# Kernel tuning notes

Measured on AMD Instinct MI355X. Metric: run time of the kernel, lower is better.

Reference implementation:

```python
import jax, jax.numpy as jnp
import numpy as np

N_NODES = 50000
N_EDGES = 1200000
NODE_DIM = 64
HIDDEN = 64
OUT_DIM = 1
N_LAYERS = 3


def setup_inputs() -> dict:
    key = jax.random.key(0)
    ks = jax.random.split(key, 16)
    inp = {
        "H": jax.random.normal(ks[0], (N_NODES, NODE_DIM), dtype=jnp.float32),
        "edge_index": jax.random.randint(ks[1], (2, N_EDGES), 0, N_NODES, dtype=jnp.int64),
        "E": jax.random.normal(ks[2], (N_EDGES, 16), dtype=jnp.float32),
    }
    # per-layer params: node_encoder (enc) and update_w (upd); weights stored [in, out]
    for i in range(N_LAYERS):
        in_dim = NODE_DIM if i == 0 else HIDDEN
        s = 1.0 / np.sqrt(in_dim)
        inp[f"enc_w{i}"] = jax.random.uniform(ks[3 + 2 * i], (in_dim, HIDDEN), jnp.float32, -s, s)
        inp[f"enc_b{i}"] = jax.random.uniform(ks[4 + 2 * i], (HIDDEN,), jnp.float32, -s, s)
        sh = 1.0 / np.sqrt(HIDDEN)
        inp[f"upd_w{i}"] = jax.random.uniform(ks[9 + 2 * i], (HIDDEN, HIDDEN), jnp.float32, -sh, sh)
        inp[f"upd_b{i}"] = jax.random.uniform(ks[10 + 2 * i], (HIDDEN,), jnp.float32, -sh, sh)
    so = 1.0 / np.sqrt(HIDDEN)
    inp["out_w"] = jax.random.uniform(ks[15], (HIDDEN, OUT_DIM), jnp.float32, -so, so)
    inp["out_b"] = jnp.zeros((OUT_DIM,), jnp.float32)
    return inp


def _gcn_forward(H, edge_index, params):
    u, v = edge_index[0], edge_index[1]
    # symmetric normalization with implicit self-loop degree bump (calc_norm_factor)
    deg = jax.ops.segment_sum(jnp.ones(u.shape[0], H.dtype), u, num_segments=N_NODES) + 1.0
    dis = deg ** -0.5  # deg >= 1, never inf
    norm = dis[u] * dis[v]  # [n_edges]
    for i in range(N_LAYERS):
        enc_w, enc_b, upd_w, upd_b = params[i]
        H = H @ enc_w + enc_b                      # node_encoder
        msgs = norm[:, None] * H[u]                # gather + scale
        agg = jax.ops.segment_sum(msgs, v, num_segments=N_NODES)  # scatter-add
        H = jax.nn.relu((agg + H) @ upd_w + upd_b)  # update + ReLU (dropout = identity in eval)
    return H


def reference(H, edge_index, E, enc_w0, enc_b0, upd_w0, upd_b0, enc_w1, enc_b1,
              upd_w1, upd_b1, enc_w2, enc_b2, upd_w2, upd_b2, out_w, out_b):
    params = [(enc_w0, enc_b0, upd_w0, upd_b0),
              (enc_w1, enc_b1, upd_w1, upd_b1),
              (enc_w2, enc_b2, upd_w2, upd_b2)]
    Hf = _gcn_forward(H, edge_index, params)
    graph_emb = jnp.mean(Hf, axis=0, keepdims=True)  # [1, HIDDEN] readout (batch=None)
    return graph_emb @ out_w + out_b                 # [1, OUT_DIM]
```

## Files before the change

### kernel.cpp

```cpp
#include <hip/hip_runtime.h>
#include <hip/hip_fp16.h>

#define NN 50000
#define NE 1200000
#define DIM 64
#define NB 782
#define SLICES 512
#define ES 2344
#define VCAP 2048
#define GB 782
#define FRONT_LDS 33792

__global__ __launch_bounds__(256) void k_fold(const float* __restrict__ E0, const float* __restrict__ e0,
                                              const float* __restrict__ U0, const float* __restrict__ ub0,
                                              const float* __restrict__ E1, const float* __restrict__ e1,
                                              const float* __restrict__ U1, const float* __restrict__ ub1,
                                              const float* __restrict__ E2, const float* __restrict__ e2,
                                              const float* __restrict__ U2, const float* __restrict__ ub2,
                                              float* __restrict__ Wp, float* __restrict__ cvec,
                                              float* __restrict__ dvec) {
    __shared__ float Es[64][64];
    __shared__ float Us[64][64];
    int i = blockIdx.x;
    const float* E  = (i == 0) ? E0  : (i == 1) ? E1  : E2;
    const float* e  = (i == 0) ? e0  : (i == 1) ? e1  : e2;
    const float* U  = (i == 0) ? U0  : (i == 1) ? U1  : U2;
    const float* ub = (i == 0) ? ub0 : (i == 1) ? ub1 : ub2;
    int t = threadIdx.x;
#pragma unroll
    for (int j = 0; j < 4; ++j) {
        int idx = t + j * 256;
        int r = idx >> 4, c = (idx & 15) << 2;
        *(float4*)&Es[r][c] = *(const float4*)&E[r * 64 + c];
        *(float4*)&Us[r][c] = *(const float4*)&U[r * 64 + c];
    }
    __syncthreads();
    int r0 = (t >> 4) * 4;
    int c0 = (t & 15) * 4;
    float acc[4][4] = {};
#pragma unroll
    for (int k = 0; k < 64; k += 4) {
        float4 b0 = *(float4*)&Us[k + 0][c0];
        float4 b1 = *(float4*)&Us[k + 1][c0];
        float4 b2 = *(float4*)&Us[k + 2][c0];
        float4 b3 = *(float4*)&Us[k + 3][c0];
#pragma unroll
        for (int q = 0; q < 4; ++q) {
            float4 av = *(float4*)&Es[r0 + q][k];
            acc[q][0] = fmaf(av.x, b0.x, fmaf(av.y, b1.x, fmaf(av.z, b2.x, fmaf(av.w, b3.x, acc[q][0]))));
            acc[q][1] = fmaf(av.x, b0.y, fmaf(av.y, b1.y, fmaf(av.z, b2.y, fmaf(av.w, b3.y, acc[q][1]))));
            acc[q][2] = fmaf(av.x, b0.z, fmaf(av.y, b1.z, fmaf(av.z, b2.z, fmaf(av.w, b3.z, acc[q][2]))));
            acc[q][3] = fmaf(av.x, b0.w, fmaf(av.y, b1.w, fmaf(av.z, b2.w, fmaf(av.w, b3.w, acc[q][3]))));
        }
    }
    float* W = Wp + i * 4096;
#pragma unroll
    for (int q = 0; q < 4; ++q)
        *(float4*)&W[(r0 + q) * 64 + c0] = make_float4(acc[q][0], acc[q][1], acc[q][2], acc[q][3]);
    if (t < 64) {
        float sc = 0.f;
        for (int k = 0; k < 64; ++k) sc = fmaf(e[k], Us[k][t], sc);
        cvec[i * 64 + t] = sc;
        dvec[i * 64 + t] = sc + ub[t];
    }
}


__device__ __forceinline__ void lsort_body(char* smem, const int* __restrict__ ei,
                                           ushort* __restrict__ usort,
                                           int* __restrict__ ebuf,
                                           int* __restrict__ lpart_u,
                                           int* __restrict__ lpart_v,
                                           int s) {
    int* hist = (int*)smem;
    int* wsum = (int*)(smem + 3136);
    ushort* sbu = (ushort*)(smem + 4160);
    int* sbv = (int*)(smem + 8848);
    int t = threadIdx.x;
    int w = t >> 6, l = t & 63;
    int e0 = s * ES, e1 = min(e0 + ES, NE), len = e1 - e0;
    int i0 = t * 4;

    int uv[10], vv[10];
#pragma unroll
    for (int j = 0; j < 10; ++j) {
        int e = e0 + t + j * 256;
        uv[j] = (e < e1) ? ei[e] : -1;
        vv[j] = (e < e1) ? ei[NE + e] : -1;
    }

    for (int i = t; i < NB; i += 256) hist[i] = 0;
    __syncthreads();
#pragma unroll
    for (int j = 0; j < 10; ++j)
        if (uv[j] >= 0) atomicAdd(&hist[uv[j] >> 6], 1);
    __syncthreads();
    {
        int h0 = (i0 + 0 < NB) ? hist[i0 + 0] : 0;
        int h1 = (i0 + 1 < NB) ? hist[i0 + 1] : 0;
        int h2 = (i0 + 2 < NB) ? hist[i0 + 2] : 0;
        int h3 = (i0 + 3 < NB) ? hist[i0 + 3] : 0;
        int p1 = h0, p2 = h0 + h1, p3 = p2 + h2, p4 = p3 + h3;
        int inc = p4;
        for (int o = 1; o < 64; o <<= 1) {
            int x = __shfl_up(inc, o, 64);
            if (l >= o) inc += x;
        }
        if (l == 63) wsum[w] = inc;
        __syncthreads();
        int base = 0;
#pragma unroll
        for (int j = 0; j < 4; ++j) if (j < w) base += wsum[j];
        int total = wsum[0] + wsum[1] + wsum[2] + wsum[3];
        int excl = base + inc - p4;
        int* lpu = lpart_u + s * (NB + 1);
        if (i0 + 0 < NB) { lpu[i0 + 0] = excl;      hist[i0 + 0] = excl; }
        if (i0 + 1 < NB) { lpu[i0 + 1] = excl + p1; hist[i0 + 1] = excl + p1; }
        if (i0 + 2 < NB) { lpu[i0 + 2] = excl + p2; hist[i0 + 2] = excl + p2; }
        if (i0 + 3 < NB) { lpu[i0 + 3] = excl + p3; hist[i0 + 3] = excl + p3; }
        if (t == 255) lpu[NB] = total;
    }
    __syncthreads();
#pragma unroll
    for (int j = 0; j < 10; ++j)
        if (uv[j] >= 0) {
            int pos = atomicAdd(&hist[uv[j] >> 6], 1);
            sbu[pos] = (ushort)uv[j];
        }
    __syncthreads();
    for (int i = t; i < len; i += 256) usort[e0 + i] = sbu[i];
    for (int i = t; i < NB; i += 256) hist[i] = 0;
    __syncthreads();

#pragma unroll
    for (int j = 0; j < 10; ++j)
        if (vv[j] >= 0) atomicAdd(&hist[vv[j] >> 6], 1);
    __syncthreads();
    {
        int h0 = (i0 + 0 < NB) ? hist[i0 + 0] : 0;
        int h1 = (i0 + 1 < NB) ? hist[i0 + 1] : 0;
        int h2 = (i0 + 2 < NB) ? hist[i0 + 2] : 0;
        int h3 = (i0 + 3 < NB) ? hist[i0 + 3] : 0;
        int p1 = h0, p2 = h0 + h1, p3 = p2 + h2, p4 = p3 + h3;
        int inc = p4;
        for (int o = 1; o < 64; o <<= 1) {
            int x = __shfl_up(inc, o, 64);
            if (l >= o) inc += x;
        }
        if (l == 63) wsum[w] = inc;
        __syncthreads();
        int base = 0;
#pragma unroll
        for (int j = 0; j < 4; ++j) if (j < w) base += wsum[j];
        int total = wsum[0] + wsum[1] + wsum[2] + wsum[3];
        int excl = base + inc - p4;
        int* lpv = lpart_v + s * (NB + 1);
        if (i0 + 0 < NB) { lpv[i0 + 0] = excl;      hist[i0 + 0] = excl; }
        if (i0 + 1 < NB) { lpv[i0 + 1] = excl + p1; hist[i0 + 1] = excl + p1; }
        if (i0 + 2 < NB) { lpv[i0 + 2] = excl + p2; hist[i0 + 2] = excl + p2; }
        if (i0 + 3 < NB) { lpv[i0 + 3] = excl + p3; hist[i0 + 3] = excl + p3; }
        if (t == 255) lpv[NB] = total;
    }
    __syncthreads();
#pragma unroll
    for (int j = 0; j < 10; ++j)
        if (vv[j] >= 0) {
            int pos = atomicAdd(&hist[vv[j] >> 6], 1);
            sbv[pos] = uv[j] | ((vv[j] & 63) << 16);
        }
    __syncthreads();
    for (int i = t; i < len; i += 256) ebuf[e0 + i] = sbv[i];
}

__device__ __forceinline__ void gemm_h_body(char* smem, int blk,
                                            const float* __restrict__ A,
                                            const float* __restrict__ W,
                                            __half* __restrict__ Ph, int M) {
    float (*As)[68] = (float(*)[68])smem;
    float (*Bs)[64] = (float(*)[64])(smem + 17408);
    int t = threadIdx.x;
    int row0 = blk * 64;
#pragma unroll
    for (int i = 0; i < 4; ++i) {
        int idx = t + i * 256;
        int r = idx >> 4, c = (idx & 15) << 2;
        float4 val = make_float4(0.f, 0.f, 0.f, 0.f);
        if (row0 + r < M) val = *(const float4*)&A[(size_t)(row0 + r) * DIM + c];
        *(float4*)&As[r][c] = val;
        *(float4*)&Bs[r][c] = *(const float4*)&W[r * DIM + c];
    }
    __syncthreads();
    int r0 = (t >> 4) * 4;
    int c0 = (t & 15) * 4;
    float acc[4][4] = {};
#pragma unroll
    for (int k = 0; k < 64; k += 4) {
        float4 b0 = *(float4*)&Bs[k + 0][c0];
        float4 b1 = *(float4*)&Bs[k + 1][c0];
        float4 b2 = *(float4*)&Bs[k + 2][c0];
        float4 b3 = *(float4*)&Bs[k + 3][c0];
#pragma unroll
        for (int i = 0; i < 4; ++i) {
            float4 av = *(float4*)&As[r0 + i][k];
            acc[i][0] = fmaf(av.x, b0.x, fmaf(av.y, b1.x, fmaf(av.z, b2.x, fmaf(av.w, b3.x, acc[i][0]))));
            acc[i][1] = fmaf(av.x, b0.y, fmaf(av.y, b1.y, fmaf(av.z, b2.y, fmaf(av.w, b3.y, acc[i][1]))));
            acc[i][2] = fmaf(av.x, b0.z, fmaf(av.y, b1.z, fmaf(av.z, b2.z, fmaf(av.w, b3.z, acc[i][2]))));
            acc[i][3] = fmaf(av.x, b0.w, fmaf(av.y, b1.w, fmaf(av.z, b2.w, fmaf(av.w, b3.w, acc[i][3]))));
        }
    }
#pragma unroll
    for (int i = 0; i < 4; ++i) {
        int r = row0 + r0 + i;
        if (r < M) {
            __half2 p0 = __floats2half2_rn(acc[i][0], acc[i][1]);
            __half2 p1 = __floats2half2_rn(acc[i][2], acc[i][3]);
            uint2 pk;
            pk.x = *(unsigned int*)&p0;
            pk.y = *(unsigned int*)&p1;
            *(uint2*)&Ph[(size_t)r * DIM + c0] = pk;
        }
    }
}

__global__ __launch_bounds__(256, 2) void k_front(const int* __restrict__ ei,
                                                  ushort* __restrict__ usort,
                                                  int* __restrict__ ebuf,
                                                  int* __restrict__ lpart_u,
                                                  int* __restrict__ lpart_v,
                                                  const float* __restrict__ A,
                                                  const float* __restrict__ Wp,
                                                  __half* __restrict__ Ph) {
    extern __shared__ char smem[];
    int b = blockIdx.x;
    if (b < 256)
        lsort_body(smem, ei, usort, ebuf, lpart_u, lpart_v, b);
    else if (b < 512)
        gemm_h_body(smem, b - 256, A, Wp, Ph, NN);
    else if (b < 768)
        lsort_body(smem, ei, usort, ebuf, lpart_u, lpart_v, b - 256);
    else
        gemm_h_body(smem, b - 512, A, Wp, Ph, NN);
}

__global__ __launch_bounds__(256) void k_prep(const ushort* __restrict__ usort,
                                              const int* __restrict__ lpart_u,
                                              const int* __restrict__ ebuf,
                                              const int* __restrict__ lpart_v,
                                              float* __restrict__ dis,
                                              ushort* __restrict__ edges,
                                              int* __restrict__ row_ptr,
                                              float* __restrict__ colsum) {
    __shared__ int cache[VCAP];
    __shared__ int cnt[64];
    __shared__ int cur[64];
    __shared__ int wsum4[4];
    __shared__ int rsum4[4];
    __shared__ int sh[64];
    int bid = blockIdx.x;
    int t = threadIdx.x, w = t >> 6, l = t & 63;
    if (bid < NB) {
        int b = bid;
        if (b == 0 && t < 64) colsum[t] = 0.f;
        if (t < 64) sh[t] = 0;
        __syncthreads();
        for (int s = t; s < SLICES; s += 256) {
            const int* row = lpart_u + s * (NB + 1);
            int st = row[b], en = row[b + 1];
            for (int i = st; i < en; ++i)
                atomicAdd(&sh[usort[s * ES + i] & 63], 1);
        }
        __syncthreads();
        int n = (b << 6) + t;
        if (t < 64 && n < NN) dis[n] = rsqrtf((float)sh[t] + 1.0f);
        return;
    }
    int b = bid - NB;
    int s0 = t * 2, s1 = t * 2 + 1;
    const int* r0p = lpart_v + s0 * (NB + 1);
    const int* r1p = lpart_v + s1 * (NB + 1);
    int a0 = r0p[b], a1 = r0p[b + 1];
    int c0 = r1p[b], c1 = r1p[b + 1];
    int len0 = a1 - a0, len1 = c1 - c0;
    int tl = len0 + len1;
    int ts = a0 + c0;
    int inc = tl;
    for (int o = 1; o < 64; o <<= 1) {
        int x = __shfl_up(inc, o, 64);
        if (l >= o) inc += x;
    }
    int tss = ts;
    for (int off = 32; off; off >>= 1) tss += __shfl_down(tss, off, 64);
    if (l == 63) wsum4[w] = inc;
    if (l == 0) rsum4[w] = tss;
    if (t < 64) cnt[t] = 0;
    __syncthreads();
    int base = 0;
#pragma unroll
    for (int j = 0; j < 4; ++j) if (j < w) base += wsum4[j];
    int n = wsum4[0] + wsum4[1] + wsum4[2] + wsum4[3];
    int rbase = rsum4[0] + rsum4[1] + rsum4[2] + rsum4[3];
    int pos = base + inc - tl;
    if (n <= VCAP) {
        for (int i = 0; i < len0; ++i) cache[pos + i] = ebuf[s0 * ES + a0 + i];
        int pos1 = pos + len0;
        for (int i = 0; i < len1; ++i) cache[pos1 + i] = ebuf[s1 * ES + c0 + i];
        __syncthreads();
        for (int i = t; i < n; i += 256)
            atomicAdd(&cnt[(cache[i] >> 16) & 63], 1);
        __syncthreads();
        if (w == 0) {
            int c = cnt[l];
            int inc2 = c;
            for (int o = 1; o < 64; o <<= 1) {
                int x = __shfl_up(inc2, o, 64);
                if (l >= o) inc2 += x;
            }
            int excl = inc2 - c;
            cur[l] = rbase + excl;
            row_ptr[(b << 6) + l] = rbase + excl;
        }
        __syncthreads();
        for (int i = t; i < n; i += 256) {
            int rec = cache[i];
            int p2 = atomicAdd(&cur[(rec >> 16) & 63], 1);
            edges[p2] = (ushort)(rec & 0xFFFF);
        }
    } else {
        for (int s = t; s < SLICES; s += 256) {
            const int* row = lpart_v + s * (NB + 1);
            int st = row[b], en = row[b + 1];
            for (int i = st; i < en; ++i)
                atomicAdd(&cnt[(ebuf[s * ES + i] >> 16) & 63], 1);
        }
        __syncthreads();
        if (w == 0) {
            int c = cnt[l];
            int inc2 = c;
            for (int o = 1; o < 64; o <<= 1) {
                int x = __shfl_up(inc2, o, 64);
                if (l >= o) inc2 += x;
            }
            int excl = inc2 - c;
            cur[l] = rbase + excl;
            row_ptr[(b << 6) + l] = rbase + excl;
        }
        __syncthreads();
        for (int s = t; s < SLICES; s += 256) {
            const int* row = lpart_v + s * (NB + 1);
            int st = row[b], en = row[b + 1];
            for (int i = st; i < en; ++i) {
                int rec = ebuf[s * ES + i];
                int p2 = atomicAdd(&cur[(rec >> 16) & 63], 1);
                edges[p2] = (ushort)(rec & 0xFFFF);
            }
        }
    }
}

__global__ __launch_bounds__(256) void k_gemm(const __half* __restrict__ Hh,
                                              const float* __restrict__ W,
                                              __half* __restrict__ Ph) {
    __shared__ float As[64][68];
    __shared__ float Bs[64][64];
    int t = threadIdx.x;
    int row0 = blockIdx.x * 64;
#pragma unroll
    for (int i = 0; i < 4; ++i) {
        int idx = t + i * 256;
        int r = idx >> 4, c = (idx & 15) << 2;
        float4 val = make_float4(0.f, 0.f, 0.f, 0.f);
        if (row0 + r < NN) {
            uint2 hv = *(const uint2*)&Hh[(size_t)(row0 + r) * DIM + c];
            float2 f0 = __half22float2(*(const __half2*)&hv.x);
            float2 f1 = __half22float2(*(const __half2*)&hv.y);
            val = make_float4(f0.x, f0.y, f1.x, f1.y);
        }
        *(float4*)&As[r][c] = val;
        *(float4*)&Bs[r][c] = *(const float4*)&W[r * DIM + c];
    }
    __syncthreads();
    int r0 = (t >> 4) * 4;
    int c0 = (t & 15) * 4;
    float acc[4][4] = {};
#pragma unroll
    for (int k = 0; k < 64; k += 4) {
        float4 b0 = *(float4*)&Bs[k + 0][c0];
        float4 b1 = *(float4*)&Bs[k + 1][c0];
        float4 b2 = *(float4*)&Bs[k + 2][c0];
        float4 b3 = *(float4*)&Bs[k + 3][c0];
#pragma unroll
        for (int i = 0; i < 4; ++i) {
            float4 av = *(float4*)&As[r0 + i][k];
            acc[i][0] = fmaf(av.x, b0.x, fmaf(av.y, b1.x, fmaf(av.z, b2.x, fmaf(av.w, b3.x, acc[i][0]))));
            acc[i][1] = fmaf(av.x, b0.y, fmaf(av.y, b1.y, fmaf(av.z, b2.y, fmaf(av.w, b3.y, acc[i][1]))));
            acc[i][2] = fmaf(av.x, b0.z, fmaf(av.y, b1.z, fmaf(av.z, b2.z, fmaf(av.w, b3.z, acc[i][2]))));
            acc[i][3] = fmaf(av.x, b0.w, fmaf(av.y, b1.w, fmaf(av.z, b2.w, fmaf(av.w, b3.w, acc[i][3]))));
        }
    }
#pragma unroll
    for (int i = 0; i < 4; ++i) {
        int r = row0 + r0 + i;
        if (r < NN) {
            __half2 p0 = __floats2half2_rn(acc[i][0], acc[i][1]);
            __half2 p1 = __floats2half2_rn(acc[i][2], acc[i][3]);
            uint2 pk;
            pk.x = *(unsigned int*)&p0;
            pk.y = *(unsigned int*)&p1;
            *(uint2*)&Ph[(size_t)r * DIM + c0] = pk;
        }
    }
}

template<bool FIRST>
__global__ __launch_bounds__(256) void k_agg(const uint4* __restrict__ Pq4,
                                             const float* __restrict__ dis,
                                             const int* __restrict__ row_ptr,
                                             const ushort* __restrict__ edges,
                                             const float* __restrict__ cvec,
                                             const float* __restrict__ dvec,
                                             float* __restrict__ s,
                                             __half* __restrict__ Hh) {
    __shared__ ushort se[4][64];
    __shared__ float swt[4][64];
    int w = threadIdx.x >> 6, l = threadIdx.x & 63;
    int node = (blockIdx.x << 2) + w;
    int start = row_ptr[node];
    int num = row_ptr[node + 1] - start;
    int g = l >> 3;
    int p = l & 7;
    float4 a0 = {0.f, 0.f, 0.f, 0.f};
    float4 a1 = {0.f, 0.f, 0.f, 0.f};
    float sw = 0.f;
    for (int base = 0; base < num; base += 64) {
        int lim = min(64, num - base);
        ushort u = 0;
        float wv = 0.f;
        if (l < lim) { u = edges[start + base + l]; wv = dis[u]; }
        se[w][l] = u;
        swt[w][l] = wv;
        __builtin_amdgcn_wave_barrier();
        int octs = (lim + 7) >> 3;
        int rr[8]; float ww[8]; uint4 hh[8];
#pragma unroll
        for (int q = 0; q < 8; ++q)
            if (q < octs) { rr[q] = se[w][8 * q + g]; ww[q] = swt[w][8 * q + g]; }
#pragma unroll
        for (int q = 0; q < 8; ++q)
            if (q < octs) hh[q] = Pq4[(rr[q] << 3) + p];
#pragma unroll
        for (int q = 0; q < 8; ++q)
            if (q < octs) {
                float wt = ww[q];
                if (FIRST) sw += wt;
                float2 f0 = __half22float2(*(const __half2*)&hh[q].x);
                float2 f1 = __half22float2(*(const __half2*)&hh[q].y);
                float2 f2 = __half22float2(*(const __half2*)&hh[q].z);
                float2 f3 = __half22float2(*(const __half2*)&hh[q].w);
                a0.x = fmaf(wt, f0.x, a0.x);
                a0.y = fmaf(wt, f0.y, a0.y);
                a0.z = fmaf(wt, f1.x, a0.z);
                a0.w = fmaf(wt, f1.y, a0.w);
                a1.x = fmaf(wt, f2.x, a1.x);
                a1.y = fmaf(wt, f2.y, a1.y);
                a1.z = fmaf(wt, f3.x, a1.z);
                a1.w = fmaf(wt, f3.y, a1.w);
            }
        __builtin_amdgcn_wave_barrier();
    }
#pragma unroll
    for (int m = 8; m < 64; m <<= 1) {
        a0.x += __shfl_xor(a0.x, m, 64);
        a0.y += __shfl_xor(a0.y, m, 64);
        a0.z += __shfl_xor(a0.z, m, 64);
        a0.w += __shfl_xor(a0.w, m, 64);
        a1.x += __shfl_xor(a1.x, m, 64);
        a1.y += __shfl_xor(a1.y, m, 64);
        a1.z += __shfl_xor(a1.z, m, 64);
        a1.w += __shfl_xor(a1.w, m, 64);
        if (FIRST) sw += __shfl_xor(sw, m, 64);
    }
    if (g == 0) {
        float dv = dis[node];
        float sv;
        if (FIRST) {
            sv = dv * sw;
            if (p == 0) s[node] = sv;
        } else {
            sv = s[node];
        }
        uint4 pv = Pq4[(node << 3) + p];
        float2 s0 = __half22float2(*(const __half2*)&pv.x);
        float2 s1 = __half22float2(*(const __half2*)&pv.y);
        float2 s2 = __half22float2(*(const __half2*)&pv.z);
        float2 s3 = __half22float2(*(const __half2*)&pv.w);
        float4 cA = *(const float4*)&cvec[p << 3];
        float4 cB = *(const float4*)&cvec[(p << 3) + 4];
        float4 dA = *(const float4*)&dvec[p << 3];
        float4 dB = *(const float4*)&dvec[(p << 3) + 4];
        float o0 = fmaxf(fmaf(dv, a0.x, s0.x) + fmaf(sv, cA.x, dA.x), 0.f);
        float o1 = fmaxf(fmaf(dv, a0.y, s0.y) + fmaf(sv, cA.y, dA.y), 0.f);
        float o2 = fmaxf(fmaf(dv, a0.z, s1.x) + fmaf(sv, cA.z, dA.z), 0.f);
        float o3 = fmaxf(fmaf(dv, a0.w, s1.y) + fmaf(sv, cA.w, dA.w), 0.f);
        float o4 = fmaxf(fmaf(dv, a1.x, s2.x) + fmaf(sv, cB.x, dB.x), 0.f);
        float o5 = fmaxf(fmaf(dv, a1.y, s2.y) + fmaf(sv, cB.y, dB.y), 0.f);
        float o6 = fmaxf(fmaf(dv, a1.z, s3.x) + fmaf(sv, cB.z, dB.z), 0.f);
        float o7 = fmaxf(fmaf(dv, a1.w, s3.y) + fmaf(sv, cB.w, dB.w), 0.f);
        __half2 h0 = __floats2half2_rn(o0, o1);
        __half2 h1 = __floats2half2_rn(o2, o3);
        __half2 h2 = __floats2half2_rn(o4, o5);
        __half2 h3 = __floats2half2_rn(o6, o7);
        uint4 pk;
        pk.x = *(unsigned int*)&h0;
        pk.y = *(unsigned int*)&h1;
        pk.z = *(unsigned int*)&h2;
        pk.w = *(unsigned int*)&h3;
        *(uint4*)&Hh[((size_t)node << 6) + (p << 3)] = pk;
    }
}

__global__ __launch_bounds__(256) void k_colsum(const __half* __restrict__ Hh,
                                                float* __restrict__ colsum) {
    __shared__ float scs[64];
    int t = threadIdx.x;
    if (t < 64) scs[t] = 0.f;
    __syncthreads();
    int p = t & 7;
    float a[8] = {};
    for (int r = blockIdx.x * 32 + (t >> 3); r < NN; r += 256 * 32) {
        uint4 hv = *(const uint4*)&Hh[((size_t)r << 6) + (p << 3)];
        float2 f0 = __half22float2(*(const __half2*)&hv.x);
        float2 f1 = __half22float2(*(const __half2*)&hv.y);
        float2 f2 = __half22float2(*(const __half2*)&hv.z);
        float2 f3 = __half22float2(*(const __half2*)&hv.w);
        a[0] += f0.x; a[1] += f0.y; a[2] += f1.x; a[3] += f1.y;
        a[4] += f2.x; a[5] += f2.y; a[6] += f3.x; a[7] += f3.y;
    }
#pragma unroll
    for (int j = 0; j < 8; ++j) atomicAdd(&scs[(p << 3) + j], a[j]);
    __syncthreads();
    if (t < 64) atomicAdd(&colsum[t], scs[t]);
}

__global__ void k_out(const float* __restrict__ colsum, const float* __restrict__ out_w,
                      const float* __restrict__ out_b, float* __restrict__ out) {
    int f = threadIdx.x;
    float v = colsum[f] * (1.0f / (float)NN) * out_w[f];
    for (int off = 32; off; off >>= 1) v += __shfl_down(v, off, 64);
    if (f == 0) out[0] = v + out_b[0];
}

extern "C" void kernel_launch(void* const* d_in, const int* in_sizes, int n_in,
                              void* d_out, int out_size, void* d_ws, size_t ws_size,
                              hipStream_t stream) {
    const float* H  = (const float*)d_in[0];
    const int*   ei = (const int*)d_in[1];
    const float* enc_w[3] = { (const float*)d_in[3], (const float*)d_in[7],  (const float*)d_in[11] };
    const float* enc_b[3] = { (const float*)d_in[4], (const float*)d_in[8],  (const float*)d_in[12] };
    const float* upd_w[3] = { (const float*)d_in[5], (const float*)d_in[9],  (const float*)d_in[13] };
    const float* upd_b[3] = { (const float*)d_in[6], (const float*)d_in[10], (const float*)d_in[14] };
    const float* out_w = (const float*)d_in[15];
    const float* out_b = (const float*)d_in[16];
    float* out = (float*)d_out;

    size_t off = 0;
    auto carve = [&](size_t bytes) {
        void* p = (char*)d_ws + off;
        off = (off + bytes + 255) & ~(size_t)255;
        return p;
    };
    int*    lpart_u = (int*)carve((size_t)SLICES * (NB + 1) * 4);
    int*    lpart_v = (int*)carve((size_t)SLICES * (NB + 1) * 4);
    float*  dis     = (float*)carve((size_t)NN * 4);
    float*  sarr    = (float*)carve((size_t)NN * 4);
    ushort* usort   = (ushort*)carve((size_t)SLICES * ES * 2);
    int*    ebuf    = (int*)carve((size_t)SLICES * ES * 4);
    ushort* edges   = (ushort*)carve((size_t)NE * 2);
    int*    row_ptr = (int*)carve((size_t)(NN + 65) * 4);
    __half* Ph      = (__half*)carve((size_t)NN * DIM * 2);
    __half* Hh      = (__half*)carve((size_t)NN * DIM * 2);
    float*  Wp      = (float*)carve(3 * 64 * 64 * 4);
    float*  cvec    = (float*)carve(3 * 64 * 4);
    float*  dvec    = (float*)carve(3 * 64 * 4);
    float*  colsum  = (float*)carve(64 * 4);

    const int AB = NN / 4;
    const uint4* Pq4 = (const uint4*)Ph;

    k_fold<<<3, 256, 0, stream>>>(enc_w[0], enc_b[0], upd_w[0], upd_b[0],
                                  enc_w[1], enc_b[1], upd_w[1], upd_b[1],
                                  enc_w[2], enc_b[2], upd_w[2], upd_b[2],
                                  Wp, cvec, dvec);
    k_front<<<512 + GB, 256, FRONT_LDS, stream>>>(ei, usort, ebuf, lpart_u, lpart_v,
                                                  H, Wp, Ph);
    k_prep<<<2 * NB, 256, 0, stream>>>(usort, lpart_u, ebuf, lpart_v,
                                       dis, edges, row_ptr, colsum);

    k_agg<true><<<AB, 256, 0, stream>>>(Pq4, dis, row_ptr, edges,
                                        cvec + 0, dvec + 0, sarr, Hh);
    k_gemm<<<GB, 256, 0, stream>>>(Hh, Wp + 4096, Ph);
    k_agg<false><<<AB, 256, 0, stream>>>(Pq4, dis, row_ptr, edges,
                                         cvec + 64, dvec + 64, sarr, Hh);
    k_gemm<<<GB, 256, 0, stream>>>(Hh, Wp + 8192, Ph);
    k_agg<false><<<AB, 256, 0, stream>>>(Pq4, dis, row_ptr, edges,
                                         cvec + 128, dvec + 128, sarr, Hh);

    k_colsum<<<256, 256, 0, stream>>>(Hh, colsum);
    k_out<<<1, 64, 0, stream>>>(colsum, out_w, out_b, out);
}
```

Baseline: 342.2 us.

## Fuse aggregation with next-layer GEMM and fold weights inside front kernel

```diff
diff --git a/kernel.cpp b/kernel.cpp
--- a/kernel.cpp
+++ b/kernel.cpp
@@ -10,22 +10,18 @@
 #define VCAP 2048
 #define GB 782
 #define FRONT_LDS 33792
-
-__global__ __launch_bounds__(256) void k_fold(const float* __restrict__ E0, const float* __restrict__ e0,
-                                              const float* __restrict__ U0, const float* __restrict__ ub0,
-                                              const float* __restrict__ E1, const float* __restrict__ e1,
-                                              const float* __restrict__ U1, const float* __restrict__ ub1,
-                                              const float* __restrict__ E2, const float* __restrict__ e2,
-                                              const float* __restrict__ U2, const float* __restrict__ ub2,
-                                              float* __restrict__ Wp, float* __restrict__ cvec,
-                                              float* __restrict__ dvec) {
-    __shared__ float Es[64][64];
-    __shared__ float Us[64][64];
-    int i = blockIdx.x;
-    const float* E  = (i == 0) ? E0  : (i == 1) ? E1  : E2;
-    const float* e  = (i == 0) ? e0  : (i == 1) ? e1  : e2;
-    const float* U  = (i == 0) ? U0  : (i == 1) ? U1  : U2;
-    const float* ub = (i == 0) ? ub0 : (i == 1) ? ub1 : ub2;
+#define FB 3125
+
+__device__ __forceinline__ void fold_body(char* smem, int i,
+                                          const float* __restrict__ E,
+                                          const float* __restrict__ e,
+                                          const float* __restrict__ U,
+                                          const float* __restrict__ ub,
+                                          float* __restrict__ Wp,
+                                          float* __restrict__ cvec,
+                                          float* __restrict__ dvec) {
+    float (*Es)[64] = (float(*)[64])smem;
+    float (*Us)[64] = (float(*)[64])(smem + 16384);
     int t = threadIdx.x;
 #pragma unroll
     for (int j = 0; j < 4; ++j) {
@@ -172,10 +168,11 @@
     for (int i = t; i < len; i += 256) ebuf[e0 + i] = sbv[i];
 }
 
-__device__ __forceinline__ void gemm_h_body(char* smem, int blk,
-                                            const float* __restrict__ A,
-                                            const float* __restrict__ W,
-                                            __half* __restrict__ Ph, int M) {
+__device__ __forceinline__ void gemm0_body(char* smem, int blk,
+                                           const float* __restrict__ H,
+                                           const float* __restrict__ E0,
+                                           const float* __restrict__ U0,
+                                           __half* __restrict__ Ph) {
     float (*As)[68] = (float(*)[68])smem;
     float (*Bs)[64] = (float(*)[64])(smem + 17408);
     int t = threadIdx.x;
@@ -185,9 +182,9 @@
         int idx = t + i * 256;
         int r = idx >> 4, c = (idx & 15) << 2;
         float4 val = make_float4(0.f, 0.f, 0.f, 0.f);
-        if (row0 + r < M) val = *(const float4*)&A[(size_t)(row0 + r) * DIM + c];
+        if (row0 + r < NN) val = *(const float4*)&H[(size_t)(row0 + r) * DIM + c];
         *(float4*)&As[r][c] = val;
-        *(float4*)&Bs[r][c] = *(const float4*)&W[r * DIM + c];
+        *(float4*)&Bs[r][c] = *(const float4*)&E0[r * DIM + c];
     }
     __syncthreads();
     int r0 = (t >> 4) * 4;
@@ -208,12 +205,39 @@
             acc[i][3] = fmaf(av.x, b0.w, fmaf(av.y, b1.w, fmaf(av.z, b2.w, fmaf(av.w, b3.w, acc[i][3]))));
         }
     }
+    __syncthreads();
+#pragma unroll
+    for (int i = 0; i < 4; ++i)
+        *(float4*)&As[r0 + i][c0] = make_float4(acc[i][0], acc[i][1], acc[i][2], acc[i][3]);
+#pragma unroll
+    for (int i = 0; i < 4; ++i) {
+        int idx = t + i * 256;
+        int r = idx >> 4, c = (idx & 15) << 2;
+        *(float4*)&Bs[r][c] = *(const float4*)&U0[r * DIM + c];
+    }
+    __syncthreads();
+    float acc2[4][4] = {};
+#pragma unroll
+    for (int k = 0; k < 64; k += 4) {
+        float4 b0 = *(float4*)&Bs[k + 0][c0];
+        float4 b1 = *(float4*)&Bs[k + 1][c0];
+        float4 b2 = *(float4*)&Bs[k + 2][c0];
+        float4 b3 = *(float4*)&Bs[k + 3][c0];
+#pragma unroll
+        for (int i = 0; i < 4; ++i) {
+            float4 av = *(float4*)&As[r0 + i][k];
+            acc2[i][0] = fmaf(av.x, b0.x, fmaf(av.y, b1.x, fmaf(av.z, b2.x, fmaf(av.w, b3.x, acc2[i][0]))));
+            acc2[i][1] = fmaf(av.x, b0.y, fmaf(av.y, b1.y, fmaf(av.z, b2.y, fmaf(av.w, b3.y, acc2[i][1]))));
+            acc2[i][2] = fmaf(av.x, b0.z, fmaf(av.y, b1.z, fmaf(av.z, b2.z, fmaf(av.w, b3.z, acc2[i][2]))));
+            acc2[i][3] = fmaf(av.x, b0.w, fmaf(av.y, b1.w, fmaf(av.z, b2.w, fmaf(av.w, b3.w, acc2[i][3]))));
+        }
+    }
 #pragma unroll
     for (int i = 0; i < 4; ++i) {
         int r = row0 + r0 + i;
-        if (r < M) {
-            __half2 p0 = __floats2half2_rn(acc[i][0], acc[i][1]);
-            __half2 p1 = __floats2half2_rn(acc[i][2], acc[i][3]);
+        if (r < NN) {
+            __half2 p0 = __floats2half2_rn(acc2[i][0], acc2[i][1]);
+            __half2 p1 = __floats2half2_rn(acc2[i][2], acc2[i][3]);
             uint2 pk;
             pk.x = *(unsigned int*)&p0;
             pk.y = *(unsigned int*)&p1;
@@ -227,19 +251,35 @@
                                                   int* __restrict__ ebuf,
                                                   int* __restrict__ lpart_u,
                                                   int* __restrict__ lpart_v,
-                                                  const float* __restrict__ A,
-                                                  const float* __restrict__ Wp,
-                                                  __half* __restrict__ Ph) {
+                                                  const float* __restrict__ H,
+                                                  const float* __restrict__ E0, const float* __restrict__ e0,
+                                                  const float* __restrict__ U0, const float* __restrict__ ub0,
+                                                  const float* __restrict__ E1, const float* __restrict__ e1,
+                                                  const float* __restrict__ U1, const float* __restrict__ ub1,
+                                                  const float* __restrict__ E2, const float* __restrict__ e2,
+                                                  const float* __restrict__ U2, const float* __restrict__ ub2,
+                                                  __half* __restrict__ Ph,
+                                                  float* __restrict__ Wp,
+                                                  float* __restrict__ cvec,
+                                                  float* __restrict__ dvec) {
     extern __shared__ char smem[];
     int b = blockIdx.x;
     if (b < 256)
         lsort_body(smem, ei, usort, ebuf, lpart_u, lpart_v, b);
     else if (b < 512)
-        gemm_h_body(smem, b - 256, A, Wp, Ph, NN);
+        gemm0_body(smem, b - 256, H, E0, U0, Ph);
     else if (b < 768)
         lsort_body(smem, ei, usort, ebuf, lpart_u, lpart_v, b - 256);
-    else
-        gemm_h_body(smem, b - 512, A, Wp, Ph, NN);
+    else if (b < 512 + GB)
+        gemm0_body(smem, b - 512, H, E0, U0, Ph);
+    else {
+        int i = b - (512 + GB);
+        const float* E  = (i == 0) ? E0  : (i == 1) ? E1  : E2;
+        const float* e  = (i == 0) ? e0  : (i == 1) ? e1  : e2;
+        const float* U  = (i == 0) ? U0  : (i == 1) ? U1  : U2;
+        const float* ub = (i == 0) ? ub0 : (i == 1) ? ub1 : ub2;
+        fold_body(smem, i, E, e, U, ub, Wp, cvec, dvec);
+    }
 }
 
 __global__ __launch_bounds__(256) void k_prep(const ushort* __restrict__ usort,
@@ -357,77 +397,19 @@
     }
 }
 
-__global__ __launch_bounds__(256) void k_gemm(const __half* __restrict__ Hh,
-                                              const float* __restrict__ W,
-                                              __half* __restrict__ Ph) {
-    __shared__ float As[64][68];
-    __shared__ float Bs[64][64];
-    int t = threadIdx.x;
-    int row0 = blockIdx.x * 64;
-#pragma unroll
-    for (int i = 0; i < 4; ++i) {
-        int idx = t + i * 256;
-        int r = idx >> 4, c = (idx & 15) << 2;
-        float4 val = make_float4(0.f, 0.f, 0.f, 0.f);
-        if (row0 + r < NN) {
-            uint2 hv = *(const uint2*)&Hh[(size_t)(row0 + r) * DIM + c];
-            float2 f0 = __half22float2(*(const __half2*)&hv.x);
-            float2 f1 = __half22float2(*(const __half2*)&hv.y);
-            val = make_float4(f0.x, f0.y, f1.x, f1.y);
-        }
-        *(float4*)&As[r][c] = val;
-        *(float4*)&Bs[r][c] = *(const float4*)&W[r * DIM + c];
-    }
-    __syncthreads();
-    int r0 = (t >> 4) * 4;
-    int c0 = (t & 15) * 4;
-    float acc[4][4] = {};
-#pragma unroll
-    for (int k = 0; k < 64; k += 4) {
-        float4 b0 = *(float4*)&Bs[k + 0][c0];
-        float4 b1 = *(float4*)&Bs[k + 1][c0];
-        float4 b2 = *(float4*)&Bs[k + 2][c0];
-        float4 b3 = *(float4*)&Bs[k + 3][c0];
-#pragma unroll
-        for (int i = 0; i < 4; ++i) {
-            float4 av = *(float4*)&As[r0 + i][k];
-            acc[i][0] = fmaf(av.x, b0.x, fmaf(av.y, b1.x, fmaf(av.z, b2.x, fmaf(av.w, b3.x, acc[i][0]))));
-            acc[i][1] = fmaf(av.x, b0.y, fmaf(av.y, b1.y, fmaf(av.z, b2.y, fmaf(av.w, b3.y, acc[i][1]))));
-            acc[i][2] = fmaf(av.x, b0.z, fmaf(av.y, b1.z, fmaf(av.z, b2.z, fmaf(av.w, b3.z, acc[i][2]))));
-            acc[i][3] = fmaf(av.x, b0.w, fmaf(av.y, b1.w, fmaf(av.z, b2.w, fmaf(av.w, b3.w, acc[i][3]))));
-        }
-    }
-#pragma unroll
-    for (int i = 0; i < 4; ++i) {
-        int r = row0 + r0 + i;
-        if (r < NN) {
-            __half2 p0 = __floats2half2_rn(acc[i][0], acc[i][1]);
-            __half2 p1 = __floats2half2_rn(acc[i][2], acc[i][3]);
-            uint2 pk;
-            pk.x = *(unsigned int*)&p0;
-            pk.y = *(unsigned int*)&p1;
-            *(uint2*)&Ph[(size_t)r * DIM + c0] = pk;
-        }
-    }
-}
-
 template<bool FIRST>
-__global__ __launch_bounds__(256) void k_agg(const uint4* __restrict__ Pq4,
-                                             const float* __restrict__ dis,
-                                             const int* __restrict__ row_ptr,
-                                             const ushort* __restrict__ edges,
-                                             const float* __restrict__ cvec,
-                                             const float* __restrict__ dvec,
-                                             float* __restrict__ s,
-                                             __half* __restrict__ Hh) {
-    __shared__ ushort se[4][64];
-    __shared__ float swt[4][64];
-    int w = threadIdx.x >> 6, l = threadIdx.x & 63;
-    int node = (blockIdx.x << 2) + w;
+__device__ __forceinline__ void agg_node(const uint4* __restrict__ Pq4,
+                                         const float* __restrict__ dis,
+                                         const int* __restrict__ row_ptr,
+                                         const ushort* __restrict__ edges,
+                                         const float* __restrict__ cvec,
+                                         const float* __restrict__ dvec,
+                                         float* __restrict__ sarr,
+                                         ushort* se, float* swt,
+                                         int node, int l, int g, int p,
+                                         float out[8]) {
     int start = row_ptr[node];
     int num = row_ptr[node + 1] - start;
-    int g = l >> 3;
-    int p = l & 7;
     float4 a0 = {0.f, 0.f, 0.f, 0.f};
     float4 a1 = {0.f, 0.f, 0.f, 0.f};
     float sw = 0.f;
@@ -436,14 +418,14 @@
         ushort u = 0;
         float wv = 0.f;
         if (l < lim) { u = edges[start + base + l]; wv = dis[u]; }
-        se[w][l] = u;
-        swt[w][l] = wv;
+        se[l] = u;
+        swt[l] = wv;
         __builtin_amdgcn_wave_barrier();
         int octs = (lim + 7) >> 3;
         int rr[8]; float ww[8]; uint4 hh[8];
 #pragma unroll
         for (int q = 0; q < 8; ++q)
-            if (q < octs) { rr[q] = se[w][8 * q + g]; ww[q] = swt[w][8 * q + g]; }
+            if (q < octs) { rr[q] = se[8 * q + g]; ww[q] = swt[8 * q + g]; }
 #pragma unroll
         for (int q = 0; q < 8; ++q)
             if (q < octs) hh[q] = Pq4[(rr[q] << 3) + p];
@@ -484,9 +466,9 @@
         float sv;
         if (FIRST) {
             sv = dv * sw;
-            if (p == 0) s[node] = sv;
+            if (p == 0) sarr[node] = sv;
         } else {
-            sv = s[node];
+            sv = sarr[node];
         }
         uint4 pv = Pq4[(node << 3) + p];
         float2 s0 = __half22float2(*(const __half2*)&pv.x);
@@ -497,18 +479,97 @@
         float4 cB = *(const float4*)&cvec[(p << 3) + 4];
         float4 dA = *(const float4*)&dvec[p << 3];
         float4 dB = *(const float4*)&dvec[(p << 3) + 4];
-        float o0 = fmaxf(fmaf(dv, a0.x, s0.x) + fmaf(sv, cA.x, dA.x), 0.f);
-        float o1 = fmaxf(fmaf(dv, a0.y, s0.y) + fmaf(sv, cA.y, dA.y), 0.f);
-        float o2 = fmaxf(fmaf(dv, a0.z, s1.x) + fmaf(sv, cA.z, dA.z), 0.f);
-        float o3 = fmaxf(fmaf(dv, a0.w, s1.y) + fmaf(sv, cA.w, dA.w), 0.f);
-        float o4 = fmaxf(fmaf(dv, a1.x, s2.x) + fmaf(sv, cB.x, dB.x), 0.f);
-        float o5 = fmaxf(fmaf(dv, a1.y, s2.y) + fmaf(sv, cB.y, dB.y), 0.f);
-        float o6 = fmaxf(fmaf(dv, a1.z, s3.x) + fmaf(sv, cB.z, dB.z), 0.f);
-        float o7 = fmaxf(fmaf(dv, a1.w, s3.y) + fmaf(sv, cB.w, dB.w), 0.f);
-        __half2 h0 = __floats2half2_rn(o0, o1);
-        __half2 h1 = __floats2half2_rn(o2, o3);
-        __half2 h2 = __floats2half2_rn(o4, o5);
-        __half2 h3 = __floats2half2_rn(o6, o7);
+        out[0] = fmaxf(fmaf(dv, a0.x, s0.x) + fmaf(sv, cA.x, dA.x), 0.f);
+        out[1] = fmaxf(fmaf(dv, a0.y, s0.y) + fmaf(sv, cA.y, dA.y), 0.f);
+        out[2] = fmaxf(fmaf(dv, a0.z, s1.x) + fmaf(sv, cA.z, dA.z), 0.f);
+        out[3] = fmaxf(fmaf(dv, a0.w, s1.y) + fmaf(sv, cA.w, dA.w), 0.f);
+        out[4] = fmaxf(fmaf(dv, a1.x, s2.x) + fmaf(sv, cB.x, dB.x), 0.f);
+        out[5] = fmaxf(fmaf(dv, a1.y, s2.y) + fmaf(sv, cB.y, dB.y), 0.f);
+        out[6] = fmaxf(fmaf(dv, a1.z, s3.x) + fmaf(sv, cB.z, dB.z), 0.f);
+        out[7] = fmaxf(fmaf(dv, a1.w, s3.y) + fmaf(sv, cB.w, dB.w), 0.f);
+    }
+}
+
+template<bool FIRST>
+__global__ __launch_bounds__(256) void k_agggemm(const uint4* __restrict__ Pq4,
+                                                 const float* __restrict__ dis,
+                                                 const int* __restrict__ row_ptr,
+                                                 const ushort* __restrict__ edges,
+                                                 const float* __restrict__ cvec,
+                                                 const float* __restrict__ dvec,
+                                                 float* __restrict__ sarr,
+                                                 const float* __restrict__ W,
+                                                 __half* __restrict__ Phout) {
+    __shared__ float As[16][68];
+    __shared__ float Bs[64][64];
+    __shared__ ushort se[4][64];
+    __shared__ float swt[4][64];
+    int t = threadIdx.x, w = t >> 6, l = t & 63;
+    int g = l >> 3, p = l & 7;
+    int node0 = blockIdx.x << 4;
+#pragma unroll
+    for (int i = 0; i < 4; ++i) {
+        int idx = t + i * 256;
+        int r = idx >> 4, c = (idx & 15) << 2;
+        *(float4*)&Bs[r][c] = *(const float4*)&W[r * 64 + c];
+    }
+#pragma unroll 1
+    for (int nn = 0; nn < 4; ++nn) {
+        int node = node0 + (w << 2) + nn;
+        float out[8];
+        agg_node<FIRST>(Pq4, dis, row_ptr, edges, cvec, dvec, sarr,
+                        se[w], swt[w], node, l, g, p, out);
+        if (g == 0) {
+            int r = (w << 2) + nn;
+            *(float4*)&As[r][p << 3] = make_float4(out[0], out[1], out[2], out[3]);
+            *(float4*)&As[r][(p << 3) + 4] = make_float4(out[4], out[5], out[6], out[7]);
+        }
+    }
+    __syncthreads();
+    int r = t >> 4;
+    int c0 = (t & 15) << 2;
+    float acc0 = 0.f, acc1 = 0.f, acc2 = 0.f, acc3 = 0.f;
+#pragma unroll
+    for (int k = 0; k < 64; k += 4) {
+        float4 b0 = *(float4*)&Bs[k + 0][c0];
+        float4 b1 = *(float4*)&Bs[k + 1][c0];
+        float4 b2 = *(float4*)&Bs[k + 2][c0];
+        float4 b3 = *(float4*)&Bs[k + 3][c0];
+        float4 av = *(float4*)&As[r][k];
+        acc0 = fmaf(av.x, b0.x, fmaf(av.y, b1.x, fmaf(av.z, b2.x, fmaf(av.w, b3.x, acc0))));
+        acc1 = fmaf(av.x, b0.y, fmaf(av.y, b1.y, fmaf(av.z, b2.y, fmaf(av.w, b3.y, acc1))));
+        acc2 = fmaf(av.x, b0.z, fmaf(av.y, b1.z, fmaf(av.z, b2.z, fmaf(av.w, b3.z, acc2))));
+        acc3 = fmaf(av.x, b0.w, fmaf(av.y, b1.w, fmaf(av.z, b2.w, fmaf(av.w, b3.w, acc3))));
+    }
+    __half2 h0 = __floats2half2_rn(acc0, acc1);
+    __half2 h1 = __floats2half2_rn(acc2, acc3);
+    uint2 pk;
+    pk.x = *(unsigned int*)&h0;
+    pk.y = *(unsigned int*)&h1;
+    *(uint2*)&Phout[(size_t)(node0 + r) * DIM + c0] = pk;
+}
+
+__global__ __launch_bounds__(256) void k_agg3(const uint4* __restrict__ Pq4,
+                                              const float* __restrict__ dis,
+                                              const int* __restrict__ row_ptr,
+                                              const ushort* __restrict__ edges,
+                                              const float* __restrict__ cvec,
+                                              const float* __restrict__ dvec,
+                                              float* __restrict__ sarr,
+                                              __half* __restrict__ Hh) {
+    __shared__ ushort se[4][64];
+    __shared__ float swt[4][64];
+    int t = threadIdx.x, w = t >> 6, l = t & 63;
+    int g = l >> 3, p = l & 7;
+    int node = (blockIdx.x << 2) + w;
+    float out[8];
+    agg_node<false>(Pq4, dis, row_ptr, edges, cvec, dvec, sarr,
+                    se[w], swt[w], node, l, g, p, out);
+    if (g == 0) {
+        __half2 h0 = __floats2half2_rn(out[0], out[1]);
+        __half2 h1 = __floats2half2_rn(out[2], out[3]);
+        __half2 h2 = __floats2half2_rn(out[4], out[5]);
+        __half2 h3 = __floats2half2_rn(out[6], out[7]);
         uint4 pk;
         pk.x = *(unsigned int*)&h0;
         pk.y = *(unsigned int*)&h1;
@@ -576,33 +637,31 @@
     int*    ebuf    = (int*)carve((size_t)SLICES * ES * 4);
     ushort* edges   = (ushort*)carve((size_t)NE * 2);
     int*    row_ptr = (int*)carve((size_t)(NN + 65) * 4);
-    __half* Ph      = (__half*)carve((size_t)NN * DIM * 2);
+    __half* PhA     = (__half*)carve((size_t)NN * DIM * 2);
+    __half* PhB     = (__half*)carve((size_t)NN * DIM * 2);
     __half* Hh      = (__half*)carve((size_t)NN * DIM * 2);
     float*  Wp      = (float*)carve(3 * 64 * 64 * 4);
     float*  cvec    = (float*)carve(3 * 64 * 4);
     float*  dvec    = (float*)carve(3 * 64 * 4);
     float*  colsum  = (float*)carve(64 * 4);
 
-    const int AB = NN / 4;
-    const uint4* Pq4 = (const uint4*)Ph;
-
-    k_fold<<<3, 256, 0, stream>>>(enc_w[0], enc_b[0], upd_w[0], upd_b[0],
-                                  enc_w[1], enc_b[1], upd_w[1], upd_b[1],
-                                  enc_w[2], enc_b[2], upd_w[2], upd_b[2],
-                                  Wp, cvec, dvec);
-    k_front<<<512 + GB, 256, FRONT_LDS, stream>>>(ei, usort, ebuf, lpart_u, lpart_v,
-                                                  H, Wp, Ph);
+    const uint4* PqA = (const uint4*)PhA;
+    const uint4* PqB = (const uint4*)PhB;
+
+    k_front<<<512 + GB + 3, 256, FRONT_LDS, stream>>>(ei, usort, ebuf, lpart_u, lpart_v, H,
+                                                      enc_w[0], enc_b[0], upd_w[0], upd_b[0],
+                                                      enc_w[1], enc_b[1], upd_w[1], upd_b[1],
+                                                      enc_w[2], enc_b[2], upd_w[2], upd_b[2],
+                                                      PhA, Wp, cvec, dvec);
     k_prep<<<2 * NB, 256, 0, stream>>>(usort, lpart_u, ebuf, lpart_v,
                                        dis, edges, row_ptr, colsum);
 
-    k_agg<true><<<AB, 256, 0, stream>>>(Pq4, dis, row_ptr, edges,
-                                        cvec + 0, dvec + 0, sarr, Hh);
-    k_gemm<<<GB, 256, 0, stream>>>(Hh, Wp + 4096, Ph);
-    k_agg<false><<<AB, 256, 0, stream>>>(Pq4, dis, row_ptr, edges,
-                                         cvec + 64, dvec + 64, sarr, Hh);
-    k_gemm<<<GB, 256, 0, stream>>>(Hh, Wp + 8192, Ph);
-    k_agg<false><<<AB, 256, 0, stream>>>(Pq4, dis, row_ptr, edges,
-                                         cvec + 128, dvec + 128, sarr, Hh);
+    k_agggemm<true><<<FB, 256, 0, stream>>>(PqA, dis, row_ptr, edges,
+                                            cvec + 0, dvec + 0, sarr, Wp + 4096, PhB);
+    k_agggemm<false><<<FB, 256, 0, stream>>>(PqB, dis, row_ptr, edges,
+                                             cvec + 64, dvec + 64, sarr, Wp + 8192, PhA);
+    k_agg3<<<NN / 4, 256, 0, stream>>>(PqA, dis, row_ptr, edges,
+                                       cvec + 128, dvec + 128, sarr, Hh);
 
     k_colsum<<<256, 256, 0, stream>>>(Hh, colsum);
     k_out<<<1, 64, 0, stream>>>(colsum, out_w, out_b, out);
```

Result: faster. 316.4 us (-7.5%).
